# Performance work log

Hardware: AMD Instinct MI355X
Metric: run time of the kernel (lower is better)

The kernel has to match this reference:

```python
import jax, jax.numpy as jnp
import numpy as np

B, T, D, H = 128, 1024, 768, 768


def setup_inputs() -> dict:
    key = jax.random.key(0)
    ks = jax.random.split(key, 5)
    scale = 1.0 / np.sqrt(H)
    return {
        "x": jax.random.normal(ks[0], (B, T, D), dtype=jnp.float32),
        "h0": jnp.zeros((1, B, H), dtype=jnp.float32),
        "c0": jnp.zeros((1, B, H), dtype=jnp.float32),
        "weight_ih": jax.random.normal(ks[1], (4 * H, D), dtype=jnp.float32) * scale,
        "weight_hh": jax.random.normal(ks[2], (4 * H, H), dtype=jnp.float32) * scale,
        "bias_ih": jax.random.normal(ks[3], (4 * H,), dtype=jnp.float32) * scale,
        "bias_hh": jax.random.normal(ks[4], (4 * H,), dtype=jnp.float32) * scale,
    }


def reference(x, h0, c0, weight_ih, weight_hh, bias_ih, bias_hh):
    # x: [B,T,D]; h0,c0: [1,B,H]; weight_ih: [4H,D]; weight_hh: [4H,H]
    # Batch the input projection once (same math as per-step matmul+bias).
    x_proj = jnp.einsum("btd,gd->tbg", x, weight_ih) + bias_ih + bias_hh  # [T,B,4H]

    def step(carry, xp_t):
        h, c = carry  # each [1,B,H]
        gates = xp_t + jnp.matmul(h, weight_hh.T)  # [1,B,4H]
        i, f, g, o = jnp.split(gates, 4, axis=2)
        i = jax.nn.sigmoid(i)
        f = jax.nn.sigmoid(f)
        g = jnp.tanh(g)
        o = jax.nn.sigmoid(o)
        cy = f * c + i * g
        hy = o * jnp.tanh(cy)
        return (hy, cy), hy[0]  # emit [B,H]

    (hT, cT), ys = jax.lax.scan(step, (h0, c0), x_proj)  # ys: [T,B,H]
    out = jnp.swapaxes(ys, 0, 1)  # [B,T,H]
    return out, (hT, cT)
```

## Files before the change

### kernel.cpp

```cpp
#include <hip/hip_runtime.h>
#include <hip/hip_bf16.h>


typedef __attribute__((ext_vector_type(8))) short short8v;
typedef __attribute__((ext_vector_type(16))) float f32x16;

constexpr int B_ = 128, T_ = 1024, D_ = 768, H_ = 768;
constexpr int NWG = 96;
constexpr int NREP = 4;

constexpr size_t FINAL_U32 = 1025ull * 16;
constexpr size_t HSLOT_SH  = 96ull * 128 * 8;
constexpr size_t HREP_OFF  = 65600;
constexpr size_t HREP_B    = (size_t)NREP * 2 * 196608;
constexpr size_t BIAS_OFF  = HREP_OFF + HREP_B;
constexpr size_t WC_OFF    = BIAS_OFF + 12288;
constexpr size_t XT_OFF    = WC_OFF + 9437184;
constexpr size_t WS_NEED   = XT_OFF + 201326592;

__device__ __forceinline__ unsigned short f2bf(float f) {
  union { float f; unsigned u; } v; v.f = f;
  unsigned r = v.u + 0x7FFF + ((v.u >> 16) & 1);
  return (unsigned short)(r >> 16);
}
__device__ __forceinline__ float sigmf(float x) { return 1.0f / (1.0f + __expf(-x)); }
__device__ __forceinline__ float tanhf_(float x) {
  float ax = fabsf(x);
  float e = __expf(-2.0f * ax);
  float t = (1.0f - e) / (1.0f + e);
  return copysignf(t, x);
}

__global__ void k_xT(const float* __restrict__ x, unsigned short* __restrict__ xTb) {
  __shared__ float tile[16][776];
  const int t = blockIdx.x;
  const int tid = threadIdx.x;
  for (int chunk = 0; chunk < 8; ++chunk) {
    #pragma unroll
    for (int i = 0; i < 12; ++i) {
      int id = i * 256 + tid;
      int bl = id / 192, d4 = id % 192;
      int b = chunk * 16 + bl;
      float4 v = *(const float4*)(x + ((size_t)b * T_ + t) * D_ + d4 * 4);
      *(float4*)&tile[bl][d4 * 4] = v;
    }
    __syncthreads();
    #pragma unroll
    for (int i = 0; i < 6; ++i) {
      int id = i * 256 + tid;
      int kb = id >> 4, bl = id & 15;
      int b = chunk * 16 + bl;
      const float* src = &tile[bl][kb * 8];
      unsigned short tmp[8];
      #pragma unroll
      for (int k = 0; k < 8; ++k) tmp[k] = f2bf(src[k]);
      *(short8v*)(xTb + (((size_t)t * 96 + kb) * 128 + b) * 8) = *(short8v*)tmp;
    }
    __syncthreads();
  }
}

__global__ void k_prep_w(const float* __restrict__ wih, const float* __restrict__ whh,
                         unsigned short* __restrict__ Wc) {
  int id  = blockIdx.x * 256 + threadIdx.x;
  int wj  = id / 6144;
  int rem = id - wj * 6144;
  int src = rem / 3072; rem -= src * 3072;
  int r   = rem / 96;
  int kcp = rem - r * 96;
  int kc  = kcp ^ (r & 15);
  int grow = (r >> 3) * H_ + wj * 8 + (r & 7);
  const float* W = (src == 0) ? whh : wih;
  const float* p = W + (size_t)grow * D_ + kc * 8;
  float4 v0 = *(const float4*)p;
  float4 v1 = *(const float4*)(p + 4);
  ushort4 o0 = {f2bf(v0.x), f2bf(v0.y), f2bf(v0.z), f2bf(v0.w)};
  ushort4 o1 = {f2bf(v1.x), f2bf(v1.y), f2bf(v1.z), f2bf(v1.w)};
  *(ushort4*)(Wc + (size_t)id * 8)     = o0;
  *(ushort4*)(Wc + (size_t)id * 8 + 4) = o1;
}

__global__ void k_prep_s(const float* __restrict__ h0,
                         const float* __restrict__ bih, const float* __restrict__ bhh,
                         unsigned short* __restrict__ hrep, float* __restrict__ bias_c,
                         unsigned* __restrict__ finalc) {
  int id = blockIdx.x * 256 + threadIdx.x;
  int b = id / 768, j = id - b * 768;
  size_t p = (size_t)(j >> 3) * 1024 + b * 8 + (j & 7);
  unsigned short v = f2bf(h0[id]);
  #pragma unroll
  for (int r = 0; r < NREP; ++r) hrep[(size_t)r * 2 * HSLOT_SH + p] = v;
  if (id < 3072) {
    int wj = id >> 5, r = id & 31;
    int grow = (r >> 3) * H_ + wj * 8 + (r & 7);
    bias_c[id] = bih[grow] + bhh[grow];
  }
  for (size_t i = id; i < FINAL_U32; i += 98304) finalc[i] = 0;
}

__launch_bounds__(256, 1)
__global__ void k_lstm(const unsigned short* __restrict__ xTb,
                       const unsigned short* __restrict__ Wc,
                       const float* __restrict__ bias_c,
                       const float* __restrict__ c0,
                       unsigned short* __restrict__ hrep,
                       unsigned* finalc,
                       float* __restrict__ out,
                       float* __restrict__ hT,
                       float* __restrict__ cT) {
  __shared__ __align__(16) unsigned short Wl[2 * 32 * 768];
  __shared__ float bias_l[32];

  const int wj   = blockIdx.x;
  const int tid  = threadIdx.x;
  const int wave = tid >> 6;
  const int lane = tid & 63;
  const int col  = lane & 31;
  const int kh   = lane >> 5;
  const int sw   = col & 15;

  {
    const short8v* s = (const short8v*)(Wc + (size_t)wj * 49152);
    short8v* d = (short8v*)Wl;
    for (int i = tid; i < 6144; i += 256) d[i] = s[i];
    if (tid < 32) bias_l[tid] = bias_c[wj * 32 + tid];
  }
  __syncthreads();

  const int bg = wave * 32 + col;
  const int jg = wj * 8 + 4 * kh;

  float c_r[4];
  {
    float4 v = *(const float4*)(c0 + (size_t)bg * H_ + jg);
    c_r[0] = v.x; c_r[1] = v.y; c_r[2] = v.z; c_r[3] = v.w;
  }

  const char* wlb = (const char*)Wl;
  const int wrow0 = col * 1536;
  const int wrow1 = 49152 + col * 1536;

  const unsigned short* rd_rep = hrep + (size_t)(wj & (NREP - 1)) * 2 * HSLOT_SH;

  float bias_r[16];
  #pragma unroll
  for (int q = 0; q < 16; ++q) bias_r[q] = bias_l[(q & 3) + 8 * (q >> 2) + 4 * kh];

  f32x16 accs[4];
  {
    #pragma unroll
    for (int q = 0; q < 16; ++q) {
      accs[0][q] = bias_r[q]; accs[1][q] = 0.f; accs[2][q] = 0.f; accs[3][q] = 0.f;
    }
    const unsigned short* xp = xTb + (size_t)kh * 1024 + bg * 8;
    #pragma unroll
    for (int f = 0; f < 48; ++f) {
      short8v w = *(const short8v*)(wlb + wrow1 + (((2 * f + kh) ^ sw) << 4));
      short8v xv = *(const short8v*)(xp + f * 2048);
      accs[f & 3] = __builtin_amdgcn_mfma_f32_32x32x16_bf16(w, xv, accs[f & 3], 0, 0, 0);
    }
  }

  for (int t = 0; t < T_; ++t) {
    if (t > 0) {
      if (wave == 0) {
        const unsigned* fp = finalc + (size_t)t * 16;
        for (;;) {
          unsigned v = __hip_atomic_load(fp, __ATOMIC_RELAXED, __HIP_MEMORY_SCOPE_AGENT);
          if (v >= (unsigned)NWG) break;
          __builtin_amdgcn_s_sleep(4);
        }
      }
      __syncthreads();
      asm volatile("" ::: "memory");
    }

    short8v hfrag[48];
    {
      const unsigned short* hp =
          rd_rep + (size_t)(t & 1) * HSLOT_SH + (size_t)kh * 1024 + bg * 8;
      #pragma unroll
      for (int f = 0; f < 48; ++f) {
        asm volatile("global_load_dwordx4 %0, %1, off sc0 sc1"
                     : "=v"(hfrag[f]) : "v"(hp + f * 2048));
      }
    }
    asm volatile("s_waitcnt vmcnt(24)" ::: "memory");
    __builtin_amdgcn_sched_barrier(0);
    #pragma unroll
    for (int f = 0; f < 24; ++f) {
      short8v w = *(const short8v*)(wlb + wrow0 + (((2 * f + kh) ^ sw) << 4));
      accs[f & 3] = __builtin_amdgcn_mfma_f32_32x32x16_bf16(w, hfrag[f], accs[f & 3], 0, 0, 0);
    }
    asm volatile("s_waitcnt vmcnt(0)" ::: "memory");
    __builtin_amdgcn_sched_barrier(0);
    #pragma unroll
    for (int f = 24; f < 48; ++f) {
      short8v w = *(const short8v*)(wlb + wrow0 + (((2 * f + kh) ^ sw) << 4));
      accs[f & 3] = __builtin_amdgcn_mfma_f32_32x32x16_bf16(w, hfrag[f], accs[f & 3], 0, 0, 0);
    }

    f32x16 g;
    #pragma unroll
    for (int q = 0; q < 16; ++q)
      g[q] = (accs[0][q] + accs[1][q]) + (accs[2][q] + accs[3][q]);

    float hnew[4];
    #pragma unroll
    for (int m = 0; m < 4; ++m) {
      float gi = g[m];
      float gf = g[4 + m];
      float gg = g[8 + m];
      float go = g[12 + m];
      float cn = sigmf(gf) * c_r[m] + sigmf(gi) * tanhf_(gg);
      c_r[m] = cn;
      hnew[m] = sigmf(go) * tanhf_(cn);
    }

    union { ushort4 s; unsigned long long u; } hv;
    hv.s = (ushort4){f2bf(hnew[0]), f2bf(hnew[1]), f2bf(hnew[2]), f2bf(hnew[3])};
    {
      size_t off = (size_t)((t + 1) & 1) * HSLOT_SH + (size_t)wj * 1024 + bg * 8 + 4 * kh;
      #pragma unroll
      for (int r = 0; r < NREP; ++r) {
        __hip_atomic_store(
            (unsigned long long*)(hrep + (size_t)r * 2 * HSLOT_SH + off),
            hv.u, __ATOMIC_RELAXED, __HIP_MEMORY_SCOPE_AGENT);
      }
    }

    asm volatile("s_waitcnt vmcnt(0)" ::: "memory");
    __syncthreads();
    if (tid == 0)
      __hip_atomic_fetch_add(finalc + (size_t)(t + 1) * 16, 1u,
                             __ATOMIC_RELAXED, __HIP_MEMORY_SCOPE_AGENT);

    float4 ov = make_float4(hnew[0], hnew[1], hnew[2], hnew[3]);
    *(float4*)(out + ((size_t)bg * T_ + t) * H_ + jg) = ov;
    if (t == T_ - 1) {
      *(float4*)(hT + (size_t)bg * H_ + jg) = ov;
      float4 cv = make_float4(c_r[0], c_r[1], c_r[2], c_r[3]);
      *(float4*)(cT + (size_t)bg * H_ + jg) = cv;
    }

    if (t + 1 < T_) {
      #pragma unroll
      for (int q = 0; q < 16; ++q) {
        accs[0][q] = bias_r[q]; accs[1][q] = 0.f; accs[2][q] = 0.f; accs[3][q] = 0.f;
      }
      const unsigned short* xp =
          xTb + (size_t)(t + 1) * 98304 + (size_t)kh * 1024 + bg * 8;
      #pragma unroll
      for (int f = 0; f < 48; ++f) {
        short8v w = *(const short8v*)(wlb + wrow1 + (((2 * f + kh) ^ sw) << 4));
        short8v xv = *(const short8v*)(xp + f * 2048);
        accs[f & 3] = __builtin_amdgcn_mfma_f32_32x32x16_bf16(w, xv, accs[f & 3], 0, 0, 0);
      }
    }
  }
}

extern "C" void kernel_launch(void* const* d_in, const int* in_sizes, int n_in,
                              void* d_out, int out_size, void* d_ws, size_t ws_size,
                              hipStream_t stream) {
  const float* x   = (const float*)d_in[0];
  const float* h0  = (const float*)d_in[1];
  const float* c0  = (const float*)d_in[2];
  const float* wih = (const float*)d_in[3];
  const float* whh = (const float*)d_in[4];
  const float* bih = (const float*)d_in[5];
  const float* bhh = (const float*)d_in[6];

  float* out = (float*)d_out;
  float* hT  = out + (size_t)B_ * T_ * H_;
  float* cT  = hT + (size_t)B_ * H_;

  if (ws_size < WS_NEED) return;

  char* ws = (char*)d_ws;
  unsigned*       finalc = (unsigned*)(ws);
  unsigned short* hrep   = (unsigned short*)(ws + HREP_OFF);
  float*          biasc  = (float*)(ws + BIAS_OFF);
  unsigned short* Wc     = (unsigned short*)(ws + WC_OFF);
  unsigned short* xTp    = (unsigned short*)(ws + XT_OFF);

  k_xT<<<dim3(T_), dim3(256), 0, stream>>>(x, xTp);
  k_prep_w<<<dim3(589824 / 256), dim3(256), 0, stream>>>(wih, whh, Wc);
  k_prep_s<<<dim3((B_ * H_) / 256), dim3(256), 0, stream>>>(h0, bih, bhh, hrep, biasc, finalc);
  k_lstm<<<dim3(NWG), dim3(256), 0, stream>>>(xTp, Wc, biasc, c0, hrep, finalc, out, hT, cT);
}
```

Before: 11.05 ms.

## Repartition LSTM work: hidden-slice x batch-quarter per block, Whh in registers

Each workgroup now owns a 32-column hidden slice for one quarter of the batch, with each wave handling 8 hidden units, instead of 8 hidden units across the full batch. The recurrent weight fragments stay resident in VGPRs and Wih is read from global/L2 every step, replacing the LDS weight copy. Each step the block cooperatively loads its batch quarter of h into LDS and syncs, and the four-way replicated h buffers are dropped in favour of a single ping-pong buffer. This cuts redundant global h reads and replica stores, but adds an LDS round trip, a barrier per step, high register pressure, and global Wih traffic on every step.

Result: slower. 24.95 ms (+125.7%).

```diff
diff --git a/kernel.cpp b/kernel.cpp
--- a/kernel.cpp
+++ b/kernel.cpp
@@ -7,15 +7,14 @@
 
 constexpr int B_ = 128, T_ = 1024, D_ = 768, H_ = 768;
 constexpr int NWG = 96;
-constexpr int NREP = 4;
 
 constexpr size_t FINAL_U32 = 1025ull * 16;
+constexpr size_t PING_OFF  = 66048;
 constexpr size_t HSLOT_SH  = 96ull * 128 * 8;
-constexpr size_t HREP_OFF  = 65600;
-constexpr size_t HREP_B    = (size_t)NREP * 2 * 196608;
-constexpr size_t BIAS_OFF  = HREP_OFF + HREP_B;
-constexpr size_t WC_OFF    = BIAS_OFF + 12288;
-constexpr size_t XT_OFF    = WC_OFF + 9437184;
+constexpr size_t BIAS_OFF  = PING_OFF + 393216;
+constexpr size_t WHH_OFF   = BIAS_OFF + 12288;
+constexpr size_t WIH_OFF   = WHH_OFF + 4718592;
+constexpr size_t XT_OFF    = WIH_OFF + 4718592;
 constexpr size_t WS_NEED   = XT_OFF + 201326592;
 
 __device__ __forceinline__ unsigned short f2bf(float f) {
@@ -60,75 +59,82 @@
   }
 }
 
-__global__ void k_prep_w(const float* __restrict__ wih, const float* __restrict__ whh,
-                         unsigned short* __restrict__ Wc) {
+__global__ void k_prep_w(const float* __restrict__ whh, const float* __restrict__ wih,
+                         unsigned short* __restrict__ Whh_img,
+                         unsigned short* __restrict__ Wih_img) {
   int id  = blockIdx.x * 256 + threadIdx.x;
-  int wj  = id / 6144;
-  int rem = id - wj * 6144;
-  int src = rem / 3072; rem -= src * 3072;
-  int r   = rem / 96;
-  int kcp = rem - r * 96;
-  int kc  = kcp ^ (r & 15);
-  int grow = (r >> 3) * H_ + wj * 8 + (r & 7);
-  const float* W = (src == 0) ? whh : wih;
+  int img = id / 294912;
+  int rem = id - img * 294912;
+  int jqw = rem / 3072;
+  int rem2 = rem - jqw * 3072;
+  int kc  = rem2 >> 5;
+  int col = rem2 & 31;
+  int grow = (col >> 3) * H_ + (jqw >> 2) * 32 + (jqw & 3) * 8 + (col & 7);
+  const float* W = img ? wih : whh;
   const float* p = W + (size_t)grow * D_ + kc * 8;
   float4 v0 = *(const float4*)p;
   float4 v1 = *(const float4*)(p + 4);
-  ushort4 o0 = {f2bf(v0.x), f2bf(v0.y), f2bf(v0.z), f2bf(v0.w)};
-  ushort4 o1 = {f2bf(v1.x), f2bf(v1.y), f2bf(v1.z), f2bf(v1.w)};
-  *(ushort4*)(Wc + (size_t)id * 8)     = o0;
-  *(ushort4*)(Wc + (size_t)id * 8 + 4) = o1;
+  unsigned short o[8] = {f2bf(v0.x), f2bf(v0.y), f2bf(v0.z), f2bf(v0.w),
+                         f2bf(v1.x), f2bf(v1.y), f2bf(v1.z), f2bf(v1.w)};
+  unsigned short* dst = (img ? Wih_img : Whh_img) + (size_t)rem * 8;
+  *(short8v*)dst = *(short8v*)o;
 }
 
 __global__ void k_prep_s(const float* __restrict__ h0,
                          const float* __restrict__ bih, const float* __restrict__ bhh,
-                         unsigned short* __restrict__ hrep, float* __restrict__ bias_c,
+                         unsigned short* __restrict__ hping,
+                         float* __restrict__ bias_img,
                          unsigned* __restrict__ finalc) {
   int id = blockIdx.x * 256 + threadIdx.x;
   int b = id / 768, j = id - b * 768;
-  size_t p = (size_t)(j >> 3) * 1024 + b * 8 + (j & 7);
-  unsigned short v = f2bf(h0[id]);
-  #pragma unroll
-  for (int r = 0; r < NREP; ++r) hrep[(size_t)r * 2 * HSLOT_SH + p] = v;
+  hping[(size_t)(j >> 3) * 1024 + b * 8 + (j & 7)] = f2bf(h0[id]);
   if (id < 3072) {
-    int wj = id >> 5, r = id & 31;
-    int grow = (r >> 3) * H_ + wj * 8 + (r & 7);
-    bias_c[id] = bih[grow] + bhh[grow];
-  }
-  for (size_t i = id; i < FINAL_U32; i += 98304) finalc[i] = 0;
+    int jqw = id >> 5, col = id & 31;
+    int grow = (col >> 3) * H_ + (jqw >> 2) * 32 + (jqw & 3) * 8 + (col & 7);
+    bias_img[id] = bih[grow] + bhh[grow];
+  }
+  if (id < (int)FINAL_U32) finalc[id] = 0;
 }
 
 __launch_bounds__(256, 1)
 __global__ void k_lstm(const unsigned short* __restrict__ xTb,
-                       const unsigned short* __restrict__ Wc,
-                       const float* __restrict__ bias_c,
+                       const unsigned short* __restrict__ Whh_img,
+                       const unsigned short* __restrict__ Wih_img,
+                       const float* __restrict__ bias_img,
                        const float* __restrict__ c0,
-                       unsigned short* __restrict__ hrep,
+                       unsigned short* __restrict__ hping,
                        unsigned* finalc,
                        float* __restrict__ out,
                        float* __restrict__ hT,
                        float* __restrict__ cT) {
-  __shared__ __align__(16) unsigned short Wl[2 * 32 * 768];
-  __shared__ float bias_l[32];
+  __shared__ __align__(16) unsigned short hbuf[96 * 32 * 8];
 
   const int wj   = blockIdx.x;
+  const int jq   = wj >> 2;
+  const int c    = wj & 3;
   const int tid  = threadIdx.x;
   const int wave = tid >> 6;
   const int lane = tid & 63;
   const int col  = lane & 31;
   const int kh   = lane >> 5;
-  const int sw   = col & 15;
-
+  const int jqw  = jq * 4 + wave;
+
+  const int bg = 32 * c + col;
+  const int jg = jq * 32 + wave * 8 + 4 * kh;
+
+  short8v whh_frag[48];
   {
-    const short8v* s = (const short8v*)(Wc + (size_t)wj * 49152);
-    short8v* d = (short8v*)Wl;
-    for (int i = tid; i < 6144; i += 256) d[i] = s[i];
-    if (tid < 32) bias_l[tid] = bias_c[wj * 32 + tid];
-  }
-  __syncthreads();
-
-  const int bg = wave * 32 + col;
-  const int jg = wj * 8 + 4 * kh;
+    const unsigned short* base = Whh_img + (size_t)jqw * 96 * 32 * 8;
+    #pragma unroll
+    for (int f = 0; f < 48; ++f)
+      whh_frag[f] = *(const short8v*)(base + (((2 * f + kh) * 32) + col) * 8);
+  }
+  const unsigned short* wih_base = Wih_img + (size_t)jqw * 96 * 32 * 8;
+
+  float bias_r[16];
+  #pragma unroll
+  for (int q = 0; q < 16; ++q)
+    bias_r[q] = bias_img[jqw * 32 + (q & 3) + 8 * (q >> 2) + 4 * kh];
 
   float c_r[4];
   {
@@ -136,27 +142,17 @@
     c_r[0] = v.x; c_r[1] = v.y; c_r[2] = v.z; c_r[3] = v.w;
   }
 
-  const char* wlb = (const char*)Wl;
-  const int wrow0 = col * 1536;
-  const int wrow1 = 49152 + col * 1536;
-
-  const unsigned short* rd_rep = hrep + (size_t)(wj & (NREP - 1)) * 2 * HSLOT_SH;
-
-  float bias_r[16];
-  #pragma unroll
-  for (int q = 0; q < 16; ++q) bias_r[q] = bias_l[(q & 3) + 8 * (q >> 2) + 4 * kh];
-
   f32x16 accs[4];
   {
     #pragma unroll
     for (int q = 0; q < 16; ++q) {
       accs[0][q] = bias_r[q]; accs[1][q] = 0.f; accs[2][q] = 0.f; accs[3][q] = 0.f;
     }
-    const unsigned short* xp = xTb + (size_t)kh * 1024 + bg * 8;
     #pragma unroll
     for (int f = 0; f < 48; ++f) {
-      short8v w = *(const short8v*)(wlb + wrow1 + (((2 * f + kh) ^ sw) << 4));
-      short8v xv = *(const short8v*)(xp + f * 2048);
+      int kc = 2 * f + kh;
+      short8v w = *(const short8v*)(wih_base + (kc * 32 + col) * 8);
+      short8v xv = *(const short8v*)(xTb + (((size_t)0 * 96 + kc) * 128 + bg) * 8);
       accs[f & 3] = __builtin_amdgcn_mfma_f32_32x32x16_bf16(w, xv, accs[f & 3], 0, 0, 0);
     }
   }
@@ -175,29 +171,30 @@
       asm volatile("" ::: "memory");
     }
 
-    short8v hfrag[48];
     {
-      const unsigned short* hp =
-          rd_rep + (size_t)(t & 1) * HSLOT_SH + (size_t)kh * 1024 + bg * 8;
-      #pragma unroll
-      for (int f = 0; f < 48; ++f) {
+      const unsigned short* hb_rd = hping + (size_t)(t & 1) * HSLOT_SH;
+      short8v tmp[12];
+      #pragma unroll
+      for (int i = 0; i < 12; ++i) {
+        int id = i * 256 + tid;
+        int kb = id >> 5, bpos = id & 31;
+        const unsigned short* p = hb_rd + ((size_t)kb * 128 + 32 * c + bpos) * 8;
         asm volatile("global_load_dwordx4 %0, %1, off sc0 sc1"
-                     : "=v"(hfrag[f]) : "v"(hp + f * 2048));
-      }
-    }
-    asm volatile("s_waitcnt vmcnt(24)" ::: "memory");
-    __builtin_amdgcn_sched_barrier(0);
-    #pragma unroll
-    for (int f = 0; f < 24; ++f) {
-      short8v w = *(const short8v*)(wlb + wrow0 + (((2 * f + kh) ^ sw) << 4));
-      accs[f & 3] = __builtin_amdgcn_mfma_f32_32x32x16_bf16(w, hfrag[f], accs[f & 3], 0, 0, 0);
-    }
-    asm volatile("s_waitcnt vmcnt(0)" ::: "memory");
-    __builtin_amdgcn_sched_barrier(0);
-    #pragma unroll
-    for (int f = 24; f < 48; ++f) {
-      short8v w = *(const short8v*)(wlb + wrow0 + (((2 * f + kh) ^ sw) << 4));
-      accs[f & 3] = __builtin_amdgcn_mfma_f32_32x32x16_bf16(w, hfrag[f], accs[f & 3], 0, 0, 0);
+                     : "=v"(tmp[i]) : "v"(p));
+      }
+      asm volatile("s_waitcnt vmcnt(0)" ::: "memory");
+      #pragma unroll
+      for (int i = 0; i < 12; ++i) {
+        int id = i * 256 + tid;
+        *(short8v*)&hbuf[(size_t)id * 8] = tmp[i];
+      }
+      __syncthreads();
+    }
+
+    #pragma unroll
+    for (int f = 0; f < 48; ++f) {
+      short8v hB = *(const short8v*)&hbuf[((2 * f + kh) * 32 + col) * 8];
+      accs[f & 3] = __builtin_amdgcn_mfma_f32_32x32x16_bf16(whh_frag[f], hB, accs[f & 3], 0, 0, 0);
     }
 
     f32x16 g;
@@ -219,15 +216,10 @@
 
     union { ushort4 s; unsigned long long u; } hv;
     hv.s = (ushort4){f2bf(hnew[0]), f2bf(hnew[1]), f2bf(hnew[2]), f2bf(hnew[3])};
-    {
-      size_t off = (size_t)((t + 1) & 1) * HSLOT_SH + (size_t)wj * 1024 + bg * 8 + 4 * kh;
-      #pragma unroll
-      for (int r = 0; r < NREP; ++r) {
-        __hip_atomic_store(
-            (unsigned long long*)(hrep + (size_t)r * 2 * HSLOT_SH + off),
-            hv.u, __ATOMIC_RELAXED, __HIP_MEMORY_SCOPE_AGENT);
-      }
-    }
+    __hip_atomic_store(
+        (unsigned long long*)(hping + (size_t)((t + 1) & 1) * HSLOT_SH +
+                              ((size_t)jqw * 128 + bg) * 8 + 4 * kh),
+        hv.u, __ATOMIC_RELAXED, __HIP_MEMORY_SCOPE_AGENT);
 
     asm volatile("s_waitcnt vmcnt(0)" ::: "memory");
     __syncthreads();
@@ -248,12 +240,12 @@
       for (int q = 0; q < 16; ++q) {
         accs[0][q] = bias_r[q]; accs[1][q] = 0.f; accs[2][q] = 0.f; accs[3][q] = 0.f;
       }
-      const unsigned short* xp =
-          xTb + (size_t)(t + 1) * 98304 + (size_t)kh * 1024 + bg * 8;
+      const unsigned short* xp = xTb + (size_t)(t + 1) * 96 * 128 * 8;
       #pragma unroll
       for (int f = 0; f < 48; ++f) {
-        short8v w = *(const short8v*)(wlb + wrow1 + (((2 * f + kh) ^ sw) << 4));
-        short8v xv = *(const short8v*)(xp + f * 2048);
+        int kc = 2 * f + kh;
+        short8v w = *(const short8v*)(wih_base + (kc * 32 + col) * 8);
+        short8v xv = *(const short8v*)(xp + ((size_t)kc * 128 + bg) * 8);
         accs[f & 3] = __builtin_amdgcn_mfma_f32_32x32x16_bf16(w, xv, accs[f & 3], 0, 0, 0);
       }
     }
@@ -279,13 +271,14 @@
 
   char* ws = (char*)d_ws;
   unsigned*       finalc = (unsigned*)(ws);
-  unsigned short* hrep   = (unsigned short*)(ws + HREP_OFF);
+  unsigned short* hping  = (unsigned short*)(ws + PING_OFF);
   float*          biasc  = (float*)(ws + BIAS_OFF);
-  unsigned short* Wc     = (unsigned short*)(ws + WC_OFF);
+  unsigned short* WhhI   = (unsigned short*)(ws + WHH_OFF);
+  unsigned short* WihI   = (unsigned short*)(ws + WIH_OFF);
   unsigned short* xTp    = (unsigned short*)(ws + XT_OFF);
 
   k_xT<<<dim3(T_), dim3(256), 0, stream>>>(x, xTp);
-  k_prep_w<<<dim3(589824 / 256), dim3(256), 0, stream>>>(wih, whh, Wc);
-  k_prep_s<<<dim3((B_ * H_) / 256), dim3(256), 0, stream>>>(h0, bih, bhh, hrep, biasc, finalc);
-  k_lstm<<<dim3(NWG), dim3(256), 0, stream>>>(xTp, Wc, biasc, c0, hrep, finalc, out, hT, cT);
-}
+  k_prep_w<<<dim3(589824 / 256), dim3(256), 0, stream>>>(whh, wih, WhhI, WihI);
+  k_prep_s<<<dim3((B_ * H_) / 256), dim3(256), 0, stream>>>(h0, bih, bhh, hping, biasc, finalc);
+  k_lstm<<<dim3(NWG), dim3(256), 0, stream>>>(xTp, WhhI, WihI, biasc, c0, hping, finalc, out, hT, cT);
+}
```

## Split each hidden-column group across two workgroups and drop h replicas

Applied to the files above, without the earlier changes.

Doubles the persistent grid from 96 to 192 workgroups of 128 threads, with each pair sharing one weight slice and splitting the batch in half. This spreads the per-step recurrent work across more CUs. The four replicated hidden-state buffers are replaced by a single ping-pong buffer, removing the extra stores per step. The output store becomes nontemporal. The catch is that the barrier now waits on 192 arrivals, so synchronisation cost rises, weight loading into LDS is duplicated, and all readers contend on one copy of h.

New measurement: 9.235 ms. -16.4%, faster.

```diff
diff --git a/kernel.cpp b/kernel.cpp
--- a/kernel.cpp
+++ b/kernel.cpp
@@ -4,16 +4,15 @@
 
 typedef __attribute__((ext_vector_type(8))) short short8v;
 typedef __attribute__((ext_vector_type(16))) float f32x16;
+typedef __attribute__((ext_vector_type(4))) float f32x4;
 
 constexpr int B_ = 128, T_ = 1024, D_ = 768, H_ = 768;
-constexpr int NWG = 96;
-constexpr int NREP = 4;
+constexpr int NWG = 192;
 
 constexpr size_t FINAL_U32 = 1025ull * 16;
+constexpr size_t PING_OFF  = 66048;
 constexpr size_t HSLOT_SH  = 96ull * 128 * 8;
-constexpr size_t HREP_OFF  = 65600;
-constexpr size_t HREP_B    = (size_t)NREP * 2 * 196608;
-constexpr size_t BIAS_OFF  = HREP_OFF + HREP_B;
+constexpr size_t BIAS_OFF  = PING_OFF + 393216;
 constexpr size_t WC_OFF    = BIAS_OFF + 12288;
 constexpr size_t XT_OFF    = WC_OFF + 9437184;
 constexpr size_t WS_NEED   = XT_OFF + 201326592;
@@ -63,13 +62,13 @@
 __global__ void k_prep_w(const float* __restrict__ wih, const float* __restrict__ whh,
                          unsigned short* __restrict__ Wc) {
   int id  = blockIdx.x * 256 + threadIdx.x;
-  int wj  = id / 6144;
-  int rem = id - wj * 6144;
+  int jg  = id / 6144;
+  int rem = id - jg * 6144;
   int src = rem / 3072; rem -= src * 3072;
   int r   = rem / 96;
   int kcp = rem - r * 96;
   int kc  = kcp ^ (r & 15);
-  int grow = (r >> 3) * H_ + wj * 8 + (r & 7);
+  int grow = (r >> 3) * H_ + jg * 8 + (r & 7);
   const float* W = (src == 0) ? whh : wih;
   const float* p = W + (size_t)grow * D_ + kc * 8;
   float4 v0 = *(const float4*)p;
@@ -82,28 +81,26 @@
 
 __global__ void k_prep_s(const float* __restrict__ h0,
                          const float* __restrict__ bih, const float* __restrict__ bhh,
-                         unsigned short* __restrict__ hrep, float* __restrict__ bias_c,
+                         unsigned short* __restrict__ hping,
+                         float* __restrict__ bias_c,
                          unsigned* __restrict__ finalc) {
   int id = blockIdx.x * 256 + threadIdx.x;
   int b = id / 768, j = id - b * 768;
-  size_t p = (size_t)(j >> 3) * 1024 + b * 8 + (j & 7);
-  unsigned short v = f2bf(h0[id]);
-  #pragma unroll
-  for (int r = 0; r < NREP; ++r) hrep[(size_t)r * 2 * HSLOT_SH + p] = v;
+  hping[(size_t)(j >> 3) * 1024 + b * 8 + (j & 7)] = f2bf(h0[id]);
   if (id < 3072) {
-    int wj = id >> 5, r = id & 31;
-    int grow = (r >> 3) * H_ + wj * 8 + (r & 7);
+    int jg = id >> 5, r = id & 31;
+    int grow = (r >> 3) * H_ + jg * 8 + (r & 7);
     bias_c[id] = bih[grow] + bhh[grow];
   }
-  for (size_t i = id; i < FINAL_U32; i += 98304) finalc[i] = 0;
-}
-
-__launch_bounds__(256, 1)
+  if (id < (int)FINAL_U32) finalc[id] = 0;
+}
+
+__launch_bounds__(128, 1)
 __global__ void k_lstm(const unsigned short* __restrict__ xTb,
                        const unsigned short* __restrict__ Wc,
                        const float* __restrict__ bias_c,
                        const float* __restrict__ c0,
-                       unsigned short* __restrict__ hrep,
+                       unsigned short* __restrict__ hping,
                        unsigned* finalc,
                        float* __restrict__ out,
                        float* __restrict__ hT,
@@ -112,6 +109,8 @@
   __shared__ float bias_l[32];
 
   const int wj   = blockIdx.x;
+  const int jgrp = wj >> 1;
+  const int half = wj & 1;
   const int tid  = threadIdx.x;
   const int wave = tid >> 6;
   const int lane = tid & 63;
@@ -120,15 +119,15 @@
   const int sw   = col & 15;
 
   {
-    const short8v* s = (const short8v*)(Wc + (size_t)wj * 49152);
+    const short8v* s = (const short8v*)(Wc + (size_t)jgrp * 49152);
     short8v* d = (short8v*)Wl;
-    for (int i = tid; i < 6144; i += 256) d[i] = s[i];
-    if (tid < 32) bias_l[tid] = bias_c[wj * 32 + tid];
+    for (int i = tid; i < 6144; i += 128) d[i] = s[i];
+    if (tid < 32) bias_l[tid] = bias_c[jgrp * 32 + tid];
   }
   __syncthreads();
 
-  const int bg = wave * 32 + col;
-  const int jg = wj * 8 + 4 * kh;
+  const int bg = (half * 2 + wave) * 32 + col;
+  const int jg = jgrp * 8 + 4 * kh;
 
   float c_r[4];
   {
@@ -139,8 +138,6 @@
   const char* wlb = (const char*)Wl;
   const int wrow0 = col * 1536;
   const int wrow1 = 49152 + col * 1536;
-
-  const unsigned short* rd_rep = hrep + (size_t)(wj & (NREP - 1)) * 2 * HSLOT_SH;
 
   float bias_r[16];
   #pragma unroll
@@ -178,7 +175,7 @@
     short8v hfrag[48];
     {
       const unsigned short* hp =
-          rd_rep + (size_t)(t & 1) * HSLOT_SH + (size_t)kh * 1024 + bg * 8;
+          hping + (size_t)(t & 1) * HSLOT_SH + (size_t)kh * 1024 + bg * 8;
       #pragma unroll
       for (int f = 0; f < 48; ++f) {
         asm volatile("global_load_dwordx4 %0, %1, off sc0 sc1"
@@ -217,17 +214,12 @@
       hnew[m] = sigmf(go) * tanhf_(cn);
     }
 
-    union { ushort4 s; unsigned long long u; } hv;
-    hv.s = (ushort4){f2bf(hnew[0]), f2bf(hnew[1]), f2bf(hnew[2]), f2bf(hnew[3])};
-    {
-      size_t off = (size_t)((t + 1) & 1) * HSLOT_SH + (size_t)wj * 1024 + bg * 8 + 4 * kh;
-      #pragma unroll
-      for (int r = 0; r < NREP; ++r) {
-        __hip_atomic_store(
-            (unsigned long long*)(hrep + (size_t)r * 2 * HSLOT_SH + off),
-            hv.u, __ATOMIC_RELAXED, __HIP_MEMORY_SCOPE_AGENT);
-      }
-    }
+    union { ushort4 sv; unsigned long long u; } hv;
+    hv.sv = (ushort4){f2bf(hnew[0]), f2bf(hnew[1]), f2bf(hnew[2]), f2bf(hnew[3])};
+    __hip_atomic_store(
+        (unsigned long long*)(hping + (size_t)((t + 1) & 1) * HSLOT_SH +
+                              (size_t)jgrp * 1024 + bg * 8 + 4 * kh),
+        hv.u, __ATOMIC_RELAXED, __HIP_MEMORY_SCOPE_AGENT);
 
     asm volatile("s_waitcnt vmcnt(0)" ::: "memory");
     __syncthreads();
@@ -235,12 +227,12 @@
       __hip_atomic_fetch_add(finalc + (size_t)(t + 1) * 16, 1u,
                              __ATOMIC_RELAXED, __HIP_MEMORY_SCOPE_AGENT);
 
-    float4 ov = make_float4(hnew[0], hnew[1], hnew[2], hnew[3]);
-    *(float4*)(out + ((size_t)bg * T_ + t) * H_ + jg) = ov;
+    f32x4 ov = {hnew[0], hnew[1], hnew[2], hnew[3]};
+    __builtin_nontemporal_store(ov, (f32x4*)(out + ((size_t)bg * T_ + t) * H_ + jg));
     if (t == T_ - 1) {
-      *(float4*)(hT + (size_t)bg * H_ + jg) = ov;
-      float4 cv = make_float4(c_r[0], c_r[1], c_r[2], c_r[3]);
-      *(float4*)(cT + (size_t)bg * H_ + jg) = cv;
+      *(f32x4*)(hT + (size_t)bg * H_ + jg) = ov;
+      f32x4 cv = {c_r[0], c_r[1], c_r[2], c_r[3]};
+      *(f32x4*)(cT + (size_t)bg * H_ + jg) = cv;
     }
 
     if (t + 1 < T_) {
@@ -279,13 +271,13 @@
 
   char* ws = (char*)d_ws;
   unsigned*       finalc = (unsigned*)(ws);
-  unsigned short* hrep   = (unsigned short*)(ws + HREP_OFF);
+  unsigned short* hping  = (unsigned short*)(ws + PING_OFF);
   float*          biasc  = (float*)(ws + BIAS_OFF);
   unsigned short* Wc     = (unsigned short*)(ws + WC_OFF);
   unsigned short* xTp    = (unsigned short*)(ws + XT_OFF);
 
   k_xT<<<dim3(T_), dim3(256), 0, stream>>>(x, xTp);
   k_prep_w<<<dim3(589824 / 256), dim3(256), 0, stream>>>(wih, whh, Wc);
-  k_prep_s<<<dim3((B_ * H_) / 256), dim3(256), 0, stream>>>(h0, bih, bhh, hrep, biasc, finalc);
-  k_lstm<<<dim3(NWG), dim3(256), 0, stream>>>(xTp, Wc, biasc, c0, hrep, finalc, out, hT, cT);
-}
+  k_prep_s<<<dim3((B_ * H_) / 256), dim3(256), 0, stream>>>(h0, bih, bhh, hping, biasc, finalc);
+  k_lstm<<<dim3(NWG), dim3(128), 0, stream>>>(xTp, Wc, biasc, c0, hping, finalc, out, hT, cT);
+}
```
